# Kernel tuning notes

Measured on AMD Instinct MI355X. Metric: run time of the kernel, lower is better.

The kernel has to match this reference:

```python
import jax, jax.numpy as jnp
import numpy as np

NUM_HEADS = 16
NUM_LANDMARKS = 64
N_ITER = 6


def iterative_inv(mat):
    # mat: (B, H, L, L) row-stochastic kernel; Newton-Schulz-style iteration
    L = mat.shape[-1]
    I = jnp.eye(L, dtype=mat.dtype)
    K = mat
    # init: V = K^T / max_j(sum_i K_ij)
    denom = jnp.max(jnp.sum(K, axis=-2), axis=-1)[:, :, None, None]
    Vm = (1.0 / denom) * jnp.swapaxes(K, -1, -2)
    for _ in range(N_ITER):
        KV = jnp.matmul(K, Vm)
        Vm = jnp.matmul(0.25 * Vm, 13.0 * I - jnp.matmul(KV, 15.0 * I - jnp.matmul(KV, 7.0 * I - KV)))
    return Vm


def setup_inputs() -> dict:
    key = jax.random.key(0)
    kq, kk, kv = jax.random.split(key, 3)
    B, N, C = 4, 4096, 1024
    return {
        "Q": jax.random.normal(kq, (B, N, C), dtype=jnp.float32),
        "K": jax.random.normal(kk, (B, N, C), dtype=jnp.float32),
        "V": jax.random.normal(kv, (B, N, C), dtype=jnp.float32),
    }


def reference(Q, K, V):
    B, N, C = Q.shape
    H, Lm = NUM_HEADS, NUM_LANDMARKS
    hd = C // H
    scale = hd ** 0.5
    # (B, H, N, hd)
    q = Q.reshape(B, N, H, hd).transpose(0, 2, 1, 3) / scale
    k = K.reshape(B, N, H, hd).transpose(0, 2, 1, 3)
    v = V.reshape(B, N, H, hd).transpose(0, 2, 1, 3)

    # landmark pooling (N divisible by Lm): mean over segments of length N//Lm
    seg = N // Lm
    k_lm = k.reshape(B, H, Lm, seg, hd).mean(axis=-2)  # (B,H,Lm,hd)
    q_lm = q.reshape(B, H, Lm, seg, hd).mean(axis=-2)  # (B,H,Lm,hd)

    kernel_1 = jax.nn.softmax(jnp.einsum('bhnd,bhld->bhnl', q, k_lm), axis=-1)   # (B,H,N,Lm)
    kernel_2 = jax.nn.softmax(jnp.einsum('bhmd,bhld->bhml', q_lm, k_lm), axis=-1)  # (B,H,Lm,Lm)
    kernel_3 = jax.nn.softmax(jnp.einsum('bhld,bhnd->bhln', q_lm, k), axis=-1)   # (B,H,Lm,N)

    out = jnp.matmul(jnp.matmul(kernel_1, iterative_inv(kernel_2)), jnp.matmul(kernel_3, v))
    return out.transpose(0, 2, 1, 3).reshape(B, N, C)
```

## Files before the change

### kernel.cpp

```cpp
#include <hip/hip_runtime.h>
#include <math.h>

#define BB 4
#define NN 4096
#define CC 1024
#define HH 16
#define HD 64
#define LM 64
#define SEG 64
#define BHN (BB*HH)
#define MATP 68
#define MATE (64*MATP)

typedef __attribute__((ext_vector_type(8))) short bf16x8;
typedef __attribute__((ext_vector_type(4))) short s16x4;
typedef __attribute__((ext_vector_type(4))) float f32x4;

__device__ __forceinline__ float shfl_sum16(float v) {
  v += __shfl_xor(v, 1, 16);
  v += __shfl_xor(v, 2, 16);
  v += __shfl_xor(v, 4, 16);
  v += __shfl_xor(v, 8, 16);
  return v;
}

__device__ __forceinline__ void split8(const float* f, bf16x8& hi, bf16x8& lo) {
#pragma unroll
  for (int i = 0; i < 8; ++i) {
    unsigned u = __builtin_bit_cast(unsigned, f[i]);
    float hf = __builtin_bit_cast(float, u & 0xFFFF0000u);
    hi[i] = (short)(u >> 16);
    float l = f[i] - hf;
    unsigned ul = __builtin_bit_cast(unsigned, l);
    lo[i] = (short)(ul >> 16);
  }
}

__device__ __forceinline__ void split4(const float* f, s16x4& hi, s16x4& lo) {
#pragma unroll
  for (int i = 0; i < 4; ++i) {
    unsigned u = __builtin_bit_cast(unsigned, f[i]);
    float hf = __builtin_bit_cast(float, u & 0xFFFF0000u);
    hi[i] = (short)(u >> 16);
    float l = f[i] - hf;
    unsigned ul = __builtin_bit_cast(unsigned, l);
    lo[i] = (short)(ul >> 16);
  }
}

__device__ __forceinline__ int planeAddr(int row, int cd) {
  int B = (row << 7) + (cd << 4);
  return B ^ ((row & 7) << 4);
}
__device__ __forceinline__ bf16x8 ldP(const short* __restrict__ P, int row, int cd) {
  return *(const bf16x8*)((const char*)P + planeAddr(row, cd));
}

__device__ __forceinline__ void xpose4(float x[4], int lane) {
  bool p1 = (lane >> 4) & 1;
  float s0 = p1 ? x[0] : x[1], s1 = p1 ? x[2] : x[3];
  float r0 = __shfl_xor(s0, 16, 64), r1 = __shfl_xor(s1, 16, 64);
  if (p1) { x[0] = r0; x[2] = r1; } else { x[1] = r0; x[3] = r1; }
  bool p2 = (lane >> 5) & 1;
  s0 = p2 ? x[0] : x[2]; s1 = p2 ? x[1] : x[3];
  r0 = __shfl_xor(s0, 32, 64); r1 = __shfl_xor(s1, 32, 64);
  if (p2) { x[0] = r0; x[1] = r1; } else { x[2] = r0; x[3] = r1; }
}

__global__ __launch_bounds__(256) void lm_kernel(
    const float* __restrict__ Q, const float* __restrict__ K,
    float* __restrict__ qlm, float* __restrict__ klm) {
  int bh = blockIdx.y; int b = bh >> 4; int h = bh & 15;
  int tid = threadIdx.x;
  int l = blockIdx.x * 4 + (tid >> 6);
  int d = tid & 63;
  const float* qbase = Q + ((size_t)b*NN + (size_t)l*SEG)*CC + h*HD + d;
  const float* kbase = K + ((size_t)b*NN + (size_t)l*SEG)*CC + h*HD + d;
  float sq = 0.f, sk = 0.f;
#pragma unroll 8
  for (int s = 0; s < SEG; ++s) {
    sq += qbase[(size_t)s*CC];
    sk += kbase[(size_t)s*CC];
  }
  qlm[(size_t)bh*4096 + l*64 + d] = sq * (1.0f/(64.0f*8.0f));
  klm[(size_t)bh*4096 + l*64 + d] = sk * (1.0f/64.0f);
}

__global__ __launch_bounds__(256, 3) void k3v_kernel(
    const float* __restrict__ K, const float* __restrict__ V,
    const float* __restrict__ qlm,
    float* __restrict__ S3, float* __restrict__ ACC3) {
  __shared__ alignas(16) short KEh[64*64], KEl[64*64];
  __shared__ alignas(16) short VtH[64*64], VtL[64*64];
  __shared__ alignas(16) float Erow[64*MATP];
  const int bh = blockIdx.y, b = bh >> 4, h = bh & 15;
  const int tile = blockIdx.x, tid = threadIdx.x;
  const int wid = tid >> 6, lane = tid & 63;
  const int lr = lane & 15, lg = lane >> 4;
  const int m0 = wid*16 + lg*4;

  bf16x8 qh[2], ql[2];
#pragma unroll
  for (int ks = 0; ks < 2; ++ks) {
    const float* qp = qlm + (size_t)bh*4096 + (wid*16 + lr)*64 + ks*32 + lg*8;
    float qf[8];
    *(float4*)&qf[0] = *(const float4*)qp;
    *(float4*)&qf[4] = *(const float4*)(qp + 4);
    split8(qf, qh[ks], ql[ks]);
  }

  f32x4 acc2[4];
#pragma unroll
  for (int t = 0; t < 4; ++t) acc2[t] = (f32x4){0.f, 0.f, 0.f, 0.f};
  float srow[4] = {0.f, 0.f, 0.f, 0.f};

  const int rk0 = tid >> 3,        ck = tid & 7;
  const int rk1 = (tid + 256) >> 3;
  const int dV  = 4*lr + lg;

  float4 gk[2][2], gv[4];

#define K3V_LOAD(SUB)                                                          \
  {                                                                            \
    const int n0_ = tile*128 + (SUB)*64;                                       \
    const float* kb0 = &K[((size_t)b*NN + n0_ + rk0)*CC + h*HD + ck*8];        \
    const float* kb1 = &K[((size_t)b*NN + n0_ + rk1)*CC + h*HD + ck*8];        \
    gk[0][0] = *(const float4*)kb0;  gk[0][1] = *(const float4*)(kb0 + 4);     \
    gk[1][0] = *(const float4*)kb1;  gk[1][1] = *(const float4*)(kb1 + 4);     \
    _Pragma("unroll")                                                          \
    for (int q = 0; q < 4; ++q) {                                              \
      int f = tid + 256*q;                                                     \
      int r = f >> 4, c4 = (f & 15) << 2;                                      \
      gv[q] = *(const float4*)&V[((size_t)b*NN + n0_ + r)*CC + h*HD + c4];     \
    }                                                                          \
  }

#define K3V_WRITE()                                                            \
  {                                                                            \
    _Pragma("unroll")                                                          \
    for (int q2 = 0; q2 < 2; ++q2) {                                           \
      float kf[8];                                                             \
      *(float4*)&kf[0] = gk[q2][0];                                            \
      *(float4*)&kf[4] = gk[q2][1];                                            \
      bf16x8 khv, klv; split8(kf, khv, klv);                                   \
      int r = q2 ? rk1 : rk0;                                                  \
      int A = planeAddr(r, ck);                                                \
      *(bf16x8*)((char*)KEh + A) = khv;                                        \
      *(bf16x8*)((char*)KEl + A) = klv;                                        \
    }                                                                          \
    _Pragma("unroll")                                                          \
    for (int q = 0; q < 4; ++q) {                                              \
      float x[4] = {gv[q].x, gv[q].y, gv[q].z, gv[q].w};                       \
      xpose4(x, lane);                                                         \
      int nb = 16*q + 4*wid;                                                   \
      s16x4 vh, vl; split4(x, vh, vl);                                         \
      int B = (dV << 7) + (nb << 1);                                           \
      B ^= (dV & 7) << 4;                                                      \
      *(s16x4*)((char*)VtH + B) = vh;                                          \
      *(s16x4*)((char*)VtL + B) = vl;                                          \
    }                                                                          \
  }

#define K3V_COMPUTE()                                                          \
  {                                                                            \
    f32x4 zacc[4];                                                             \
    _Pragma("unroll")                                                          \
    for (int t = 0; t < 4; ++t) zacc[t] = (f32x4){0.f, 0.f, 0.f, 0.f};        \
    _Pragma("unroll")                                                          \
    for (int ks = 0; ks < 2; ++ks) {                                           \
      _Pragma("unroll")                                                        \
      for (int tn = 0; tn < 4; ++tn) {                                         \
        bf16x8 bh_ = ldP(KEh, tn*16 + lr, 4*ks + lg);                          \
        bf16x8 bl_ = ldP(KEl, tn*16 + lr, 4*ks + lg);                          \
        zacc[tn] = __builtin_amdgcn_mfma_f32_16x16x32_bf16(qh[ks], bh_, zacc[tn], 0, 0, 0); \
        zacc[tn] = __builtin_amdgcn_mfma_f32_16x16x32_bf16(qh[ks], bl_, zacc[tn], 0, 0, 0); \
        zacc[tn] = __builtin_amdgcn_mfma_f32_16x16x32_bf16(ql[ks], bh_, zacc[tn], 0, 0, 0); \
      }                                                                        \
    }                                                                          \
    float e[4][4];                                                             \
    _Pragma("unroll")                                                          \
    for (int tn = 0; tn < 4; ++tn)                                             \
      _Pragma("unroll")                                                        \
      for (int r = 0; r < 4; ++r) e[tn][r] = __expf(zacc[tn][r]);              \
    _Pragma("unroll")                                                          \
    for (int r = 0; r < 4; ++r) {                                              \
      float t = e[0][r] + e[1][r] + e[2][r] + e[3][r];                         \
      srow[r] += shfl_sum16(t);                                                \
    }                                                                          \
    _Pragma("unroll")                                                          \
    for (int tn = 0; tn < 4; ++tn) {                                           \
      const int n = tn*16 + lr;                                                \
      _Pragma("unroll")                                                        \
      for (int r = 0; r < 4; ++r) Erow[(m0 + r)*MATP + n] = e[tn][r];          \
    }                                                                          \
    _Pragma("unroll")                                                          \
    for (int ks = 0; ks < 2; ++ks) {                                           \
      float fa[8];                                                             \
      const float* ap = Erow + (wid*16 + lr)*MATP + ks*32 + lg*8;              \
      *(float4*)&fa[0] = *(const float4*)ap;                                   \
      *(float4*)&fa[4] = *(const float4*)(ap + 4);                             \
      bf16x8 ah, al; split8(fa, ah, al);                                       \
      _Pragma("unroll")                                                        \
      for (int tn = 0; tn < 4; ++tn) {                                         \
        bf16x8 bh_ = ldP(VtH, tn*16 + lr, 4*ks + lg);                          \
        bf16x8 bl_ = ldP(VtL, tn*16 + lr, 4*ks + lg);                          \
        acc2[tn] = __builtin_amdgcn_mfma_f32_16x16x32_bf16(ah, bh_, acc2[tn], 0, 0, 0); \
        acc2[tn] = __builtin_amdgcn_mfma_f32_16x16x32_bf16(ah, bl_, acc2[tn], 0, 0, 0); \
        acc2[tn] = __builtin_amdgcn_mfma_f32_16x16x32_bf16(al, bh_, acc2[tn], 0, 0, 0); \
      }                                                                        \
    }                                                                          \
  }

  K3V_LOAD(0)
  K3V_WRITE()
  __syncthreads();
  K3V_LOAD(1)
  K3V_COMPUTE()
  __syncthreads();
  K3V_WRITE()
  __syncthreads();
  K3V_COMPUTE()

  if (lr == 0) {
#pragma unroll
    for (int r = 0; r < 4; ++r)
      atomicAdd(&S3[bh*64 + m0 + r], srow[r]);
  }
#pragma unroll
  for (int tn = 0; tn < 4; ++tn)
#pragma unroll
    for (int r = 0; r < 4; ++r)
      atomicAdd(&ACC3[(size_t)bh*4096 + (m0 + r)*64 + tn*16 + lr], acc2[tn][r]);
}

template<bool FUSE, bool HR, bool HC, bool HG>
__device__ __forceinline__ void mm_mfma(
    const float* __restrict__ Arow, const float* __restrict__ Scol,
    float diagc, float scale,
    float* __restrict__ OutRow, float* __restrict__ OutCol, float* __restrict__ OutGlob,
    int wr, int tn, int lane) {
  const int lr = lane & 15, lg = lane >> 4;
  f32x4 acc = (f32x4){0.f, 0.f, 0.f, 0.f};

#pragma unroll
  for (int ks = 0; ks < 2; ++ks) {
    const int kb = ks*32 + lg*8;
    float fa[8];
    const float* ap = Arow + (wr*16 + lr)*MATP + kb;
    *(float4*)&fa[0] = *(const float4*)ap;
    *(float4*)&fa[4] = *(const float4*)(ap + 4);
    bf16x8 ah, al; split8(fa, ah, al);
    float fb[8];
    const float* bp = Scol + (tn*16 + lr)*MATP + kb;
    *(float4*)&fb[0] = *(const float4*)bp;
    *(float4*)&fb[4] = *(const float4*)(bp + 4);
    if (FUSE) {
      int diff = (tn*16 + lr) - kb;
#pragma unroll
      for (int i = 0; i < 8; ++i) fb[i] = (i == diff ? diagc : 0.f) - fb[i];
    }
    bf16x8 bh_, bl_; split8(fb, bh_, bl_);
    acc = __builtin_amdgcn_mfma_f32_16x16x32_bf16(ah, bh_, acc, 0, 0, 0);
    acc = __builtin_amdgcn_mfma_f32_16x16x32_bf16(ah, bl_, acc, 0, 0, 0);
    acc = __builtin_amdgcn_mfma_f32_16x16x32_bf16(al, bh_, acc, 0, 0, 0);
  }
  __syncthreads();
  const int n = tn*16 + lr, m0 = wr*16 + lg*4;
  float v0 = scale*acc[0], v1 = scale*acc[1], v2 = scale*acc[2], v3 = scale*acc[3];
  if (HC) *(float4*)&OutCol[n*MATP + m0] = make_float4(v0, v1, v2, v3);
  if (HR) {
    OutRow[(m0+0)*MATP + n] = v0;
    OutRow[(m0+1)*MATP + n] = v1;
    OutRow[(m0+2)*MATP + n] = v2;
    OutRow[(m0+3)*MATP + n] = v3;
  }
  if (HG) {
    OutGlob[(m0+0)*64 + n] = v0;
    OutGlob[(m0+1)*64 + n] = v1;
    OutGlob[(m0+2)*64 + n] = v2;
    OutGlob[(m0+3)*64 + n] = v3;
  }
  __syncthreads();
}

__global__ __launch_bounds__(1024, 1) void inv_kernel(
    const float* __restrict__ qlm, const float* __restrict__ klm,
    const float* __restrict__ S3, const float* __restrict__ ACC3,
    float* __restrict__ W) {
  extern __shared__ float sm[];
  float* K2row = sm;
  float* Vmrow = sm + 1*MATE;
  float* Vmcol = sm + 2*MATE;
  float* Xrow  = sm + 3*MATE;
  float* Xcol  = sm + 4*MATE;
  float* Ycol  = sm + 5*MATE;
  float* Zcol  = sm + 6*MATE;
  float* rs    = sm + 7*MATE;
  float* rinv  = rs + 256;
  float* red   = rinv + 64;
  const int bh = blockIdx.x, tid = threadIdx.x;
  const int wid = tid >> 6, lane = tid & 63;
  const int wr = wid & 3, tn = wid >> 2;
  const int lr = lane & 15, lg = lane >> 4;
  const int m0 = wr*16 + lg*4, n = tn*16 + lr;

  {
    int f = tid, r = f >> 4, c4 = (f & 15) << 2;
    *(float4*)&Xrow[r*MATP + c4] = *(const float4*)&qlm[(size_t)bh*4096 + f*4];
    *(float4*)&Xcol[r*MATP + c4] = *(const float4*)&klm[(size_t)bh*4096 + f*4];
  }
  __syncthreads();

  {
    f32x4 zacc = (f32x4){0.f, 0.f, 0.f, 0.f};
#pragma unroll
    for (int ks = 0; ks < 2; ++ks) {
      const int kb = ks*32 + lg*8;
      float fa[8];
      const float* ap = Xrow + (wr*16 + lr)*MATP + kb;
      *(float4*)&fa[0] = *(const float4*)ap;
      *(float4*)&fa[4] = *(const float4*)(ap + 4);
      bf16x8 ah, al; split8(fa, ah, al);
      float fb[8];
      const float* bp = Xcol + (tn*16 + lr)*MATP + kb;
      *(float4*)&fb[0] = *(const float4*)bp;
      *(float4*)&fb[4] = *(const float4*)(bp + 4);
      bf16x8 bh_, bl_; split8(fb, bh_, bl_);
      zacc = __builtin_amdgcn_mfma_f32_16x16x32_bf16(ah, bh_, zacc, 0, 0, 0);
      zacc = __builtin_amdgcn_mfma_f32_16x16x32_bf16(ah, bl_, zacc, 0, 0, 0);
      zacc = __builtin_amdgcn_mfma_f32_16x16x32_bf16(al, bh_, zacc, 0, 0, 0);
    }
    float e[4];
#pragma unroll
    for (int r = 0; r < 4; ++r) e[r] = __expf(zacc[r]);
    float part[4];
#pragma unroll
    for (int r = 0; r < 4; ++r) part[r] = shfl_sum16(e[r]);
    if (lr == 0) {
#pragma unroll
      for (int r = 0; r < 4; ++r) rs[(m0 + r)*4 + tn] = part[r];
    }
    __syncthreads();
    if (tid < 64)
      rinv[tid] = 1.0f / (rs[tid*4] + rs[tid*4+1] + rs[tid*4+2] + rs[tid*4+3]);
    __syncthreads();
#pragma unroll
    for (int r = 0; r < 4; ++r)
      K2row[(m0+r)*MATP + n] = e[r] * rinv[m0 + r];
  }
  __syncthreads();

  if (tid < 64) {
    float c = 0.f;
#pragma unroll 8
    for (int i = 0; i < 64; ++i) c += K2row[i*MATP + tid];
#pragma unroll
    for (int m = 1; m < 64; m <<= 1) c = fmaxf(c, __shfl_xor(c, m, 64));
    if (tid == 0) red[0] = 1.0f / c;
  }
  __syncthreads();
  const float invden = red[0];

  {
    int f = tid, i = f >> 4, c4 = (f & 15) << 2;
    float4 kv = *(const float4*)&K2row[i*MATP + c4];
    kv.x *= invden; kv.y *= invden; kv.z *= invden; kv.w *= invden;
    *(float4*)&Vmcol[i*MATP + c4] = kv;
    Vmrow[(c4+0)*MATP + i] = kv.x;
    Vmrow[(c4+1)*MATP + i] = kv.y;
    Vmrow[(c4+2)*MATP + i] = kv.z;
    Vmrow[(c4+3)*MATP + i] = kv.w;
  }
  __syncthreads();

  for (int it = 0; it < 6; ++it) {
    mm_mfma<false, true,  true,  false>(K2row, Vmcol, 0.f,  1.0f,  Xrow, Xcol, nullptr, wr, tn, lane);
    mm_mfma<true,  false, true,  false>(Xrow,  Xcol,  7.f,  1.0f,  nullptr, Ycol, nullptr, wr, tn, lane);
    mm_mfma<true,  false, true,  false>(Xrow,  Ycol,  15.f, 1.0f,  nullptr, Zcol, nullptr, wr, tn, lane);
    mm_mfma<true,  true,  true,  false>(Vmrow, Zcol,  13.f, 0.25f, Vmrow, Vmcol, nullptr, wr, tn, lane);
  }

  {
    int f = tid, k = f >> 4, c4 = (f & 15) << 2;
    float4 tv = *(const float4*)&ACC3[(size_t)bh*4096 + f*4];
    float ri = 1.0f / S3[bh*64 + k];
    Ycol[(c4+0)*MATP + k] = tv.x * ri;
    Ycol[(c4+1)*MATP + k] = tv.y * ri;
    Ycol[(c4+2)*MATP + k] = tv.z * ri;
    Ycol[(c4+3)*MATP + k] = tv.w * ri;
  }
  __syncthreads();
  mm_mfma<false, false, false, true>(Vmrow, Ycol, 0.f, 1.0f, nullptr, nullptr, W + (size_t)bh*4096, wr, tn, lane);
}

__global__ __launch_bounds__(256, 3) void out_kernel(
    const float* __restrict__ Q, const float* __restrict__ klm,
    const float* __restrict__ W, float* __restrict__ Out) {
  __shared__ alignas(16) short KlH[64*64], KlL[64*64];
  __shared__ alignas(16) short WtH[64*64], WtL[64*64];
  __shared__ alignas(16) float Prow[64*MATP];
  const int bh = blockIdx.y, b = bh >> 4, h = bh & 15;
  const int n0 = blockIdx.x * 64;
  const int tid = threadIdx.x;
  const int wid = tid >> 6, lane = tid & 63;
  const int lr = lane & 15, lg = lane >> 4;
  const int m0 = wid*16 + lg*4;

#pragma unroll
  for (int q2 = 0; q2 < 2; ++q2) {
    int f = tid + 256*q2;
    int r = f >> 3, c = f & 7;
    const float* kp = &klm[(size_t)bh*4096 + r*64 + c*8];
    float kf[8];
    *(float4*)&kf[0] = *(const float4*)kp;
    *(float4*)&kf[4] = *(const float4*)(kp + 4);
    bf16x8 khv, klv; split8(kf, khv, klv);
    int A = planeAddr(r, c);
    *(bf16x8*)((char*)KlH + A) = khv;
    *(bf16x8*)((char*)KlL + A) = klv;
  }
  const int dW = 4*lr + lg;
#pragma unroll
  for (int q = 0; q < 4; ++q) {
    int f = tid + 256*q;
    int r = f >> 4, c4 = (f & 15) << 2;
    float4 wv = *(const float4*)&W[(size_t)bh*4096 + r*64 + c4];
    float x[4] = {wv.x, wv.y, wv.z, wv.w};
    xpose4(x, lane);
    int nb = 16*q + 4*wid;
    s16x4 wh, wl; split4(x, wh, wl);
    int B = (dW << 7) + (nb << 1);
    B ^= (dW & 7) << 4;
    *(s16x4*)((char*)WtH + B) = wh;
    *(s16x4*)((char*)WtL + B) = wl;
  }

  bf16x8 qh[2], qlo[2];
#pragma unroll
  for (int ks = 0; ks < 2; ++ks) {
    const float* qp = Q + ((size_t)b*NN + n0 + wid*16 + lr)*CC + h*HD + ks*32 + lg*8;
    float qf[8];
    *(float4*)&qf[0] = *(const float4*)qp;
    *(float4*)&qf[4] = *(const float4*)(qp + 4);
#pragma unroll
    for (int i = 0; i < 8; ++i) qf[i] *= 0.125f;
    split8(qf, qh[ks], qlo[ks]);
  }
  __syncthreads();

  f32x4 zacc[4];
#pragma unroll
  for (int t = 0; t < 4; ++t) zacc[t] = (f32x4){0.f, 0.f, 0.f, 0.f};
#pragma unroll
  for (int ks = 0; ks < 2; ++ks) {
#pragma unroll
    for (int tn = 0; tn < 4; ++tn) {
      bf16x8 bh_ = ldP(KlH, tn*16 + lr, 4*ks + lg);
      bf16x8 bl_ = ldP(KlL, tn*16 + lr, 4*ks + lg);
      zacc[tn] = __builtin_amdgcn_mfma_f32_16x16x32_bf16(qh[ks], bh_, zacc[tn], 0, 0, 0);
      zacc[tn] = __builtin_amdgcn_mfma_f32_16x16x32_bf16(qh[ks], bl_, zacc[tn], 0, 0, 0);
      zacc[tn] = __builtin_amdgcn_mfma_f32_16x16x32_bf16(qlo[ks], bh_, zacc[tn], 0, 0, 0);
    }
  }
  float e[4][4];
#pragma unroll
  for (int tn = 0; tn < 4; ++tn)
#pragma unroll
    for (int r = 0; r < 4; ++r) e[tn][r] = __expf(zacc[tn][r]);
#pragma unroll
  for (int r = 0; r < 4; ++r) {
    float t = e[0][r] + e[1][r] + e[2][r] + e[3][r];
    t = shfl_sum16(t);
    float ri = 1.0f / t;
#pragma unroll
    for (int tn = 0; tn < 4; ++tn) e[tn][r] *= ri;
  }
#pragma unroll
  for (int tn = 0; tn < 4; ++tn) {
    const int n = tn*16 + lr;
#pragma unroll
    for (int r = 0; r < 4; ++r) Prow[(m0+r)*MATP + n] = e[tn][r];
  }

  f32x4 oacc[4];
#pragma unroll
  for (int t = 0; t < 4; ++t) oacc[t] = (f32x4){0.f, 0.f, 0.f, 0.f};
#pragma unroll
  for (int ks = 0; ks < 2; ++ks) {
    float fa[8];
    const float* ap = Prow + (wid*16 + lr)*MATP + ks*32 + lg*8;
    *(float4*)&fa[0] = *(const float4*)ap;
    *(float4*)&fa[4] = *(const float4*)(ap + 4);
    bf16x8 ah, al; split8(fa, ah, al);
#pragma unroll
    for (int tn = 0; tn < 4; ++tn) {
      bf16x8 bh_ = ldP(WtH, tn*16 + lr, 4*ks + lg);
      bf16x8 bl_ = ldP(WtL, tn*16 + lr, 4*ks + lg);
      oacc[tn] = __builtin_amdgcn_mfma_f32_16x16x32_bf16(ah, bh_, oacc[tn], 0, 0, 0);
      oacc[tn] = __builtin_amdgcn_mfma_f32_16x16x32_bf16(ah, bl_, oacc[tn], 0, 0, 0);
      oacc[tn] = __builtin_amdgcn_mfma_f32_16x16x32_bf16(al, bh_, oacc[tn], 0, 0, 0);
    }
  }
#pragma unroll
  for (int tn = 0; tn < 4; ++tn) {
    const int d = tn*16 + lr;
#pragma unroll
    for (int r = 0; r < 4; ++r)
      Out[((size_t)b*NN + n0 + m0 + r)*CC + h*HD + d] = oacc[tn][r];
  }
}

extern "C" void kernel_launch(void* const* d_in, const int* in_sizes, int n_in,
                              void* d_out, int out_size, void* d_ws, size_t ws_size,
                              hipStream_t stream) {
  const float* Q = (const float*)d_in[0];
  const float* K = (const float*)d_in[1];
  const float* V = (const float*)d_in[2];
  float* out = (float*)d_out;
  float* ws  = (float*)d_ws;

  float* qlm  = ws;
  float* klm  = ws + 262144;
  float* S3   = ws + 524288;
  float* ACC3 = ws + 528384;
  float* Wm   = ws + 790528;

  size_t shC = (size_t)(7*MATE + 384)*sizeof(float);
  hipFuncSetAttribute((const void*)inv_kernel,
                      hipFuncAttributeMaxDynamicSharedMemorySize, (int)shC);

  hipMemsetAsync(S3, 0, (4096 + 262144)*sizeof(float), stream);

  lm_kernel <<<dim3(16, BHN), 256, 0, stream>>>(Q, K, qlm, klm);
  k3v_kernel<<<dim3(32, BHN), 256, 0, stream>>>(K, V, qlm, S3, ACC3);
  inv_kernel<<<dim3(BHN),    1024, shC, stream>>>(qlm, klm, S3, ACC3, Wm);
  out_kernel<<<dim3(64, BHN), 256, 0, stream>>>(Q, klm, Wm, out);
}
```

Before: 141.0 us.

## Drop K low-plane in k3v, enlarge per-block tiles, load landmark keys directly in out_kernel

In k3v_kernel, K is rounded to a single bf16 plane with round-to-nearest instead of a hi/lo split, which removes one MFMA and one LDS plane per product. The softmax staging buffer becomes a byte-addressed swizzled layout. Each block now handles 256 rows in four sub-tiles, so half as many blocks are launched. In out_kernel the landmark-key LDS staging and its barrier are removed, and keys are read from global and split in registers. Launch bounds are raised to 4 waves per SIMD for both kernels, which trades accuracy of the first-stage logits for less compute and LDS traffic.

```diff
diff --git a/kernel.cpp b/kernel.cpp
--- a/kernel.cpp
+++ b/kernel.cpp
@@ -46,6 +46,17 @@
     unsigned ul = __builtin_bit_cast(unsigned, l);
     lo[i] = (short)(ul >> 16);
   }
+}
+
+__device__ __forceinline__ bf16x8 rtn8(const float* f) {
+  bf16x8 h;
+#pragma unroll
+  for (int i = 0; i < 8; ++i) {
+    unsigned u = __builtin_bit_cast(unsigned, f[i]);
+    u += 0x7FFFu + ((u >> 16) & 1u);
+    h[i] = (short)(u >> 16);
+  }
+  return h;
 }
 
 __device__ __forceinline__ int planeAddr(int row, int cd) {
@@ -86,18 +97,19 @@
   klm[(size_t)bh*4096 + l*64 + d] = sk * (1.0f/64.0f);
 }
 
-__global__ __launch_bounds__(256, 3) void k3v_kernel(
+__global__ __launch_bounds__(256, 4) void k3v_kernel(
     const float* __restrict__ K, const float* __restrict__ V,
     const float* __restrict__ qlm,
     float* __restrict__ S3, float* __restrict__ ACC3) {
-  __shared__ alignas(16) short KEh[64*64], KEl[64*64];
+  __shared__ alignas(16) short KEh[64*64];
   __shared__ alignas(16) short VtH[64*64], VtL[64*64];
-  __shared__ alignas(16) float Erow[64*MATP];
+  __shared__ alignas(16) char  Ebuf[16384];
   const int bh = blockIdx.y, b = bh >> 4, h = bh & 15;
   const int tile = blockIdx.x, tid = threadIdx.x;
   const int wid = tid >> 6, lane = tid & 63;
   const int lr = lane & 15, lg = lane >> 4;
   const int m0 = wid*16 + lg*4;
+  const int dV = 4*lr + lg;
 
   bf16x8 qh[2], ql[2];
 #pragma unroll
@@ -114,15 +126,13 @@
   for (int t = 0; t < 4; ++t) acc2[t] = (f32x4){0.f, 0.f, 0.f, 0.f};
   float srow[4] = {0.f, 0.f, 0.f, 0.f};
 
-  const int rk0 = tid >> 3,        ck = tid & 7;
-  const int rk1 = (tid + 256) >> 3;
-  const int dV  = 4*lr + lg;
-
+  const int rk0 = tid >> 3, ck = tid & 7;
+  const int rk1 = rk0 + 32;
   float4 gk[2][2], gv[4];
 
 #define K3V_LOAD(SUB)                                                          \
   {                                                                            \
-    const int n0_ = tile*128 + (SUB)*64;                                       \
+    const int n0_ = tile*256 + (SUB)*64;                                       \
     const float* kb0 = &K[((size_t)b*NN + n0_ + rk0)*CC + h*HD + ck*8];        \
     const float* kb1 = &K[((size_t)b*NN + n0_ + rk1)*CC + h*HD + ck*8];        \
     gk[0][0] = *(const float4*)kb0;  gk[0][1] = *(const float4*)(kb0 + 4);     \
@@ -142,11 +152,9 @@
       float kf[8];                                                             \
       *(float4*)&kf[0] = gk[q2][0];                                            \
       *(float4*)&kf[4] = gk[q2][1];                                            \
-      bf16x8 khv, klv; split8(kf, khv, klv);                                   \
+      bf16x8 khv = rtn8(kf);                                                   \
       int r = q2 ? rk1 : rk0;                                                  \
-      int A = planeAddr(r, ck);                                                \
-      *(bf16x8*)((char*)KEh + A) = khv;                                        \
-      *(bf16x8*)((char*)KEl + A) = klv;                                        \
+      *(bf16x8*)((char*)KEh + planeAddr(r, ck)) = khv;                         \
     }                                                                          \
     _Pragma("unroll")                                                          \
     for (int q = 0; q < 4; ++q) {                                              \
@@ -163,6 +171,7 @@
 
 #define K3V_COMPUTE()                                                          \
   {                                                                            \
+                                 \
     f32x4 zacc[4];                                                             \
     _Pragma("unroll")                                                          \
     for (int t = 0; t < 4; ++t) zacc[t] = (f32x4){0.f, 0.f, 0.f, 0.f};        \
@@ -171,34 +180,40 @@
       _Pragma("unroll")                                                        \
       for (int tn = 0; tn < 4; ++tn) {                                         \
         bf16x8 bh_ = ldP(KEh, tn*16 + lr, 4*ks + lg);                          \
-        bf16x8 bl_ = ldP(KEl, tn*16 + lr, 4*ks + lg);                          \
         zacc[tn] = __builtin_amdgcn_mfma_f32_16x16x32_bf16(qh[ks], bh_, zacc[tn], 0, 0, 0); \
-        zacc[tn] = __builtin_amdgcn_mfma_f32_16x16x32_bf16(qh[ks], bl_, zacc[tn], 0, 0, 0); \
         zacc[tn] = __builtin_amdgcn_mfma_f32_16x16x32_bf16(ql[ks], bh_, zacc[tn], 0, 0, 0); \
       }                                                                        \
     }                                                                          \
-    float e[4][4];                                                             \
+    float ee[4][4];                                                            \
     _Pragma("unroll")                                                          \
     for (int tn = 0; tn < 4; ++tn)                                             \
       _Pragma("unroll")                                                        \
-      for (int r = 0; r < 4; ++r) e[tn][r] = __expf(zacc[tn][r]);              \
+      for (int r = 0; r < 4; ++r) ee[tn][r] = __expf(zacc[tn][r]);             \
     _Pragma("unroll")                                                          \
     for (int r = 0; r < 4; ++r) {                                              \
-      float t = e[0][r] + e[1][r] + e[2][r] + e[3][r];                         \
+      float t = ee[0][r] + ee[1][r] + ee[2][r] + ee[3][r];                     \
       srow[r] += shfl_sum16(t);                                                \
     }                                                                          \
+     \
     _Pragma("unroll")                                                          \
     for (int tn = 0; tn < 4; ++tn) {                                           \
-      const int n = tn*16 + lr;                                                \
       _Pragma("unroll")                                                        \
-      for (int r = 0; r < 4; ++r) Erow[(m0 + r)*MATP + n] = e[tn][r];          \
-    }                                                                          \
+      for (int r = 0; r < 4; ++r) {                                            \
+        int row = m0 + r;                                                      \
+        int byte = row*256 + (tn*16 + lr)*4;                                   \
+        byte ^= (row & 7) << 4;                                                \
+        *(float*)(Ebuf + byte) = ee[tn][r];                                    \
+      }                                                                        \
+    }                                                                          \
+                                   \
     _Pragma("unroll")                                                          \
     for (int ks = 0; ks < 2; ++ks) {                                           \
+      int row = wid*16 + lr;                                                   \
+      int swz = (row & 7) << 4;                                                \
+      int base = row*256 + ks*128 + lg*32;                                     \
       float fa[8];                                                             \
-      const float* ap = Erow + (wid*16 + lr)*MATP + ks*32 + lg*8;              \
-      *(float4*)&fa[0] = *(const float4*)ap;                                   \
-      *(float4*)&fa[4] = *(const float4*)(ap + 4);                             \
+      *(float4*)&fa[0] = *(const float4*)(Ebuf + (base ^ swz));                \
+      *(float4*)&fa[4] = *(const float4*)(Ebuf + ((base + 16) ^ swz));         \
       bf16x8 ah, al; split8(fa, ah, al);                                       \
       _Pragma("unroll")                                                        \
       for (int tn = 0; tn < 4; ++tn) {                                         \
@@ -215,6 +230,16 @@
   K3V_WRITE()
   __syncthreads();
   K3V_LOAD(1)
+  K3V_COMPUTE()
+  __syncthreads();
+  K3V_WRITE()
+  __syncthreads();
+  K3V_LOAD(2)
+  K3V_COMPUTE()
+  __syncthreads();
+  K3V_WRITE()
+  __syncthreads();
+  K3V_LOAD(3)
   K3V_COMPUTE()
   __syncthreads();
   K3V_WRITE()
@@ -393,10 +418,9 @@
   mm_mfma<false, false, false, true>(Vmrow, Ycol, 0.f, 1.0f, nullptr, nullptr, W + (size_t)bh*4096, wr, tn, lane);
 }
 
-__global__ __launch_bounds__(256, 3) void out_kernel(
+__global__ __launch_bounds__(256, 4) void out_kernel(
     const float* __restrict__ Q, const float* __restrict__ klm,
     const float* __restrict__ W, float* __restrict__ Out) {
-  __shared__ alignas(16) short KlH[64*64], KlL[64*64];
   __shared__ alignas(16) short WtH[64*64], WtL[64*64];
   __shared__ alignas(16) float Prow[64*MATP];
   const int bh = blockIdx.y, b = bh >> 4, h = bh & 15;
@@ -406,19 +430,6 @@
   const int lr = lane & 15, lg = lane >> 4;
   const int m0 = wid*16 + lg*4;
 
-#pragma unroll
-  for (int q2 = 0; q2 < 2; ++q2) {
-    int f = tid + 256*q2;
-    int r = f >> 3, c = f & 7;
-    const float* kp = &klm[(size_t)bh*4096 + r*64 + c*8];
-    float kf[8];
-    *(float4*)&kf[0] = *(const float4*)kp;
-    *(float4*)&kf[4] = *(const float4*)(kp + 4);
-    bf16x8 khv, klv; split8(kf, khv, klv);
-    int A = planeAddr(r, c);
-    *(bf16x8*)((char*)KlH + A) = khv;
-    *(bf16x8*)((char*)KlL + A) = klv;
-  }
   const int dW = 4*lr + lg;
 #pragma unroll
   for (int q = 0; q < 4; ++q) {
@@ -446,21 +457,28 @@
     for (int i = 0; i < 8; ++i) qf[i] *= 0.125f;
     split8(qf, qh[ks], qlo[ks]);
   }
-  __syncthreads();
 
   f32x4 zacc[4];
 #pragma unroll
   for (int t = 0; t < 4; ++t) zacc[t] = (f32x4){0.f, 0.f, 0.f, 0.f};
 #pragma unroll
-  for (int ks = 0; ks < 2; ++ks) {
-#pragma unroll
-    for (int tn = 0; tn < 4; ++tn) {
-      bf16x8 bh_ = ldP(KlH, tn*16 + lr, 4*ks + lg);
-      bf16x8 bl_ = ldP(KlL, tn*16 + lr, 4*ks + lg);
-      zacc[tn] = __builtin_amdgcn_mfma_f32_16x16x32_bf16(qh[ks], bh_, zacc[tn], 0, 0, 0);
-      zacc[tn] = __builtin_amdgcn_mfma_f32_16x16x32_bf16(qh[ks], bl_, zacc[tn], 0, 0, 0);
-      zacc[tn] = __builtin_amdgcn_mfma_f32_16x16x32_bf16(qlo[ks], bh_, zacc[tn], 0, 0, 0);
-    }
+  for (int tn = 0; tn < 4; ++tn) {
+    const float* kp = &klm[(size_t)bh*4096 + (tn*16 + lr)*64 + lg*8];
+    float4 k00 = *(const float4*)kp;
+    float4 k01 = *(const float4*)(kp + 4);
+    float4 k10 = *(const float4*)(kp + 32);
+    float4 k11 = *(const float4*)(kp + 36);
+    float kf[8];
+    *(float4*)&kf[0] = k00; *(float4*)&kf[4] = k01;
+    bf16x8 b0h, b0l; split8(kf, b0h, b0l);
+    *(float4*)&kf[0] = k10; *(float4*)&kf[4] = k11;
+    bf16x8 b1h, b1l; split8(kf, b1h, b1l);
+    zacc[tn] = __builtin_amdgcn_mfma_f32_16x16x32_bf16(qh[0], b0h, zacc[tn], 0, 0, 0);
+    zacc[tn] = __builtin_amdgcn_mfma_f32_16x16x32_bf16(qh[0], b0l, zacc[tn], 0, 0, 0);
+    zacc[tn] = __builtin_amdgcn_mfma_f32_16x16x32_bf16(qlo[0], b0h, zacc[tn], 0, 0, 0);
+    zacc[tn] = __builtin_amdgcn_mfma_f32_16x16x32_bf16(qh[1], b1h, zacc[tn], 0, 0, 0);
+    zacc[tn] = __builtin_amdgcn_mfma_f32_16x16x32_bf16(qh[1], b1l, zacc[tn], 0, 0, 0);
+    zacc[tn] = __builtin_amdgcn_mfma_f32_16x16x32_bf16(qlo[1], b1h, zacc[tn], 0, 0, 0);
   }
   float e[4][4];
 #pragma unroll
@@ -481,6 +499,7 @@
 #pragma unroll
     for (int r = 0; r < 4; ++r) Prow[(m0+r)*MATP + n] = e[tn][r];
   }
+  __syncthreads();
 
   f32x4 oacc[4];
 #pragma unroll
@@ -532,7 +551,7 @@
   hipMemsetAsync(S3, 0, (4096 + 262144)*sizeof(float), stream);
 
   lm_kernel <<<dim3(16, BHN), 256, 0, stream>>>(Q, K, qlm, klm);
-  k3v_kernel<<<dim3(32, BHN), 256, 0, stream>>>(K, V, qlm, S3, ACC3);
+  k3v_kernel<<<dim3(16, BHN), 256, 0, stream>>>(K, V, qlm, S3, ACC3);
   inv_kernel<<<dim3(BHN),    1024, shC, stream>>>(qlm, klm, S3, ACC3, Wm);
   out_kernel<<<dim3(64, BHN), 256, 0, stream>>>(Q, klm, Wm, out);
 }
```

Result: slower. 147.9 us (+4.9%).
